# Kernel optimization log

Measured on AMD Instinct MI355X. Metric: run time of the kernel, lower is better.

The kernel has to match this reference:

```python
import jax, jax.numpy as jnp
import numpy as np

W = 8       # token width
H = 2       # attention heads
NC = 1024   # number of cycles
L = 256     # darts per cycle
CLAMP = 10000.0


def _safe(x, clamp=CLAMP):
    x = jnp.nan_to_num(x, nan=0.0, posinf=clamp, neginf=-clamp)
    return jnp.clip(x, -clamp, clamp)


def _safe_softmax(logits, axis):
    w = jax.nn.softmax(_safe(logits), axis=axis)
    w = jnp.nan_to_num(w, nan=0.0, posinf=0.0, neginf=0.0)
    denom = jnp.maximum(w.sum(axis=axis, keepdims=True), 1e-6)
    return w / denom


def _layernorm(x, g, b, eps=1e-5):
    mu = x.mean(-1, keepdims=True)
    var = x.var(-1, keepdims=True)  # biased, matches torch LayerNorm
    return (x - mu) * jax.lax.rsqrt(var + eps) * g + b


def _mha(x, in_w, in_b, out_w, out_b, n_heads, mask=None):
    # torch nn.MultiheadAttention (batch_first) semantics. x: [B,S,E]
    B, S, E = x.shape
    d = E // n_heads
    qkv = x @ in_w.T + in_b
    q, k, v = jnp.split(qkv, 3, axis=-1)
    q = q.reshape(B, S, n_heads, d)
    k = k.reshape(B, S, n_heads, d)
    v = v.reshape(B, S, n_heads, d)
    scores = jnp.einsum('bshd,bthd->bhst', q, k) / jnp.sqrt(jnp.asarray(d, x.dtype))
    if mask is not None:
        scores = scores + mask  # broadcast [S,S] over batch/heads
    attn = jax.nn.softmax(scores, axis=-1)
    out = jnp.einsum('bhst,bthd->bshd', attn, v).reshape(B, S, E)
    return out @ out_w.T + out_b


def _cycle_mask(length):
    m = jnp.full((length, length), -1e9, dtype=jnp.float32)
    i = jnp.arange(length)
    m = m.at[i, i].set(0.0)
    m = m.at[i, (i - 1) % length].set(0.0)
    m = m.at[i, (i + 1) % length].set(0.0)
    return m


def _normalize_orientation(darts):
    # darts: [L,2]; polygon vertices are cumulative sums (origin first, last dart dropped)
    verts = jnp.concatenate([jnp.zeros((1, 2), darts.dtype), jnp.cumsum(darts[:-1], axis=0)], axis=0)
    x, y = verts[:, 0], verts[:, 1]
    area = 0.5 * jnp.sum(x * jnp.roll(y, -1) - y * jnp.roll(x, -1))
    return jnp.where(area >= 0.0, darts, jnp.flip(-darts, axis=0))


def setup_inputs() -> dict:
    key = jax.random.key(0)
    ks = jax.random.split(key, 32)
    def p(i, shape, s=0.2):
        return jax.random.normal(ks[i], shape, jnp.float32) * s
    return {
        'dart_features': jax.random.normal(ks[0], (NC, L, 3), jnp.float32),
        # dart_embed Linear(3,W)
        'de_w': p(1, (W, 3)), 'de_b': p(2, (W,)),
        # cycle_attn MultiheadAttention(W, 2)
        'ca_in_w': p(3, (3 * W, W)), 'ca_in_b': p(4, (3 * W,)),
        'ca_out_w': p(5, (W, W)), 'ca_out_b': p(6, (W,)),
        # cycle_norm
        'cn_g': jnp.ones((W,), jnp.float32), 'cn_b': jnp.zeros((W,), jnp.float32),
        # cycle_score Linear(W,1)
        'cs_w': p(7, (1, W)), 'cs_b': p(8, (1,)),
        # cycle_pool_proj: LN, Linear, ReLU, Linear
        'cp_ln_g': jnp.ones((W,), jnp.float32), 'cp_ln_b': jnp.zeros((W,), jnp.float32),
        'cp_w1': p(9, (W, W)), 'cp_b1': p(10, (W,)),
        'cp_w2': p(11, (W, W)), 'cp_b2': p(12, (W,)),
        # inter_cycle_attn
        'ia_in_w': p(13, (3 * W, W)), 'ia_in_b': p(14, (3 * W,)),
        'ia_out_w': p(15, (W, W)), 'ia_out_b': p(16, (W,)),
        # inter_cycle_norm
        'in_g': jnp.ones((W,), jnp.float32), 'in_b': jnp.zeros((W,), jnp.float32),
        # inter_cycle_score
        'is_w': p(17, (1, W)), 'is_b': p(18, (1,)),
        # token_proj: LN, Linear, ReLU, Linear
        'tp_ln_g': jnp.ones((W,), jnp.float32), 'tp_ln_b': jnp.zeros((W,), jnp.float32),
        'tp_w1': p(19, (W, W)), 'tp_b1': p(20, (W,)),
        'tp_w2': p(21, (W, W)), 'tp_b2': p(22, (W,)),
    }


def reference(dart_features, de_w, de_b, ca_in_w, ca_in_b, ca_out_w, ca_out_b,
              cn_g, cn_b, cs_w, cs_b, cp_ln_g, cp_ln_b, cp_w1, cp_b1, cp_w2, cp_b2,
              ia_in_w, ia_in_b, ia_out_w, ia_out_b, in_g, in_b, is_w, is_b,
              tp_ln_g, tp_ln_b, tp_w1, tp_b1, tp_w2, tp_b2):
    nc, ln, _ = dart_features.shape
    # ---- encode_cycle, vectorized over all cycles ----
    xy = jax.vmap(_normalize_orientation)(dart_features[..., :2])          # [C,L,2]
    nrm = jnp.linalg.norm(xy, axis=-1, keepdims=True)
    feats = _safe(jnp.concatenate([xy, nrm], axis=-1))                     # [C,L,3]
    emb = _safe(jax.nn.relu(feats @ de_w.T + de_b))                        # [C,L,W]
    mask = _cycle_mask(ln)
    attn = _mha(emb, ca_in_w, ca_in_b, ca_out_w, ca_out_b, H, mask)
    emb = _safe(_layernorm(_safe(emb + attn), cn_g, cn_b))                 # [C,L,W]
    logits = _safe((emb @ cs_w.T + cs_b)[..., 0])                          # [C,L]
    wts = _safe_softmax(logits, axis=1)
    pooled = jnp.sum(emb * wts[..., None], axis=1)                         # [C,W]
    hpool = _layernorm(pooled, cp_ln_g, cp_ln_b)
    cyc = _safe(jax.nn.relu(hpool @ cp_w1.T + cp_b1) @ cp_w2.T + cp_b2)    # [C,W]
    # ---- tokenize_collection ----
    coll = _safe(cyc)[None]                                                # [1,C,W]
    attn2 = _mha(coll, ia_in_w, ia_in_b, ia_out_w, ia_out_b, H)
    coll = _safe(_layernorm(_safe(coll + attn2), in_g, in_b))[0]           # [C,W]
    lg = _safe((coll @ is_w.T + is_b)[..., 0])                             # [C]
    w2 = _safe_softmax(lg, axis=0)
    tok_in = jnp.sum(coll * w2[:, None], axis=0)                           # [W]
    h2 = _layernorm(tok_in, tp_ln_g, tp_ln_b)
    token = _safe(jax.nn.relu(h2 @ tp_w1.T + tp_b1) @ tp_w2.T + tp_b2)     # [W]
    return token
```

## Files before the change

kernel.cpp:

```cpp
#include <hip/hip_runtime.h>
#include <math.h>

#define FCLAMP 10000.0f
#define LQ 256
#define NCYC 1024
#define WDIM 8

__device__ __forceinline__ float safef(float x) {
    if (isnan(x)) return 0.0f;
    x = fminf(x, FCLAMP);
    x = fmaxf(x, -FCLAMP);
    return x;
}

__device__ __forceinline__ float wsum_b(float v) {
#pragma unroll
    for (int m = 1; m <= 32; m <<= 1) v += __shfl_xor(v, m, 64);
    return v;
}
__device__ __forceinline__ float wmax_b(float v) {
#pragma unroll
    for (int m = 1; m <= 32; m <<= 1) v = fmaxf(v, __shfl_xor(v, m, 64));
    return v;
}

__global__ __launch_bounds__(LQ) void k_cycle(
    const float* __restrict__ df,
    const float* __restrict__ de_w, const float* __restrict__ de_b,
    const float* __restrict__ ca_in_w, const float* __restrict__ ca_in_b,
    const float* __restrict__ ca_out_w, const float* __restrict__ ca_out_b,
    const float* __restrict__ cn_g, const float* __restrict__ cn_b,
    const float* __restrict__ cs_w, const float* __restrict__ cs_b,
    const float* __restrict__ cp_ln_g, const float* __restrict__ cp_ln_b,
    const float* __restrict__ cp_w1, const float* __restrict__ cp_b1,
    const float* __restrict__ cp_w2, const float* __restrict__ cp_b2,
    const float* __restrict__ ia_in_w, const float* __restrict__ ia_in_b,
    float* __restrict__ ws_cyc,
    float* __restrict__ ws_q,
    float* __restrict__ ws_kT,
    float* __restrict__ ws_vT)
{
    __shared__ float sdx[LQ], sdy[LQ];
    __shared__ float sk[LQ][9], sv[LQ][9];
    __shared__ float swx[4], swy[4];
    __shared__ float sredA[4], sredB[4];
    __shared__ float spool[4][WDIM];

    const int tid  = threadIdx.x;
    const int nc   = blockIdx.x;
    const int lane = tid & 63;
    const int wid  = tid >> 6;

    const float* base = df + (size_t)nc * (LQ * 3);
    const float dx = base[tid * 3 + 0];
    const float dy = base[tid * 3 + 1];
    sdx[tid] = dx; sdy[tid] = dy;

    float ix = dx, iy = dy;
#pragma unroll
    for (int off = 1; off < 64; off <<= 1) {
        const float tx = __shfl_up(ix, off, 64);
        const float ty = __shfl_up(iy, off, 64);
        if (lane >= off) { ix += tx; iy += ty; }
    }
    if (lane == 63) { swx[wid] = ix; swy[wid] = iy; }
    __syncthreads();
    float ox = 0.f, oy = 0.f;
    for (int w = 0; w < wid; ++w) { ox += swx[w]; oy += swy[w]; }
    const float vx = ox + ix - dx;
    const float vy = oy + iy - dy;
    float c = (tid < LQ - 1) ? (vx * dy - vy * dx) : 0.f;
    float s = wsum_b(c);
    if (lane == 0) sredA[wid] = s;
    __syncthreads();
    const float area2 = sredA[0] + sredA[1] + sredA[2] + sredA[3];
    const bool flip = !(area2 >= 0.f);

    float xx, yy;
    if (flip) { xx = -sdx[LQ - 1 - tid]; yy = -sdy[LQ - 1 - tid]; }
    else      { xx =  dx;                yy =  dy; }

    const float fx = safef(xx);
    const float fy = safef(yy);
    const float fn = safef(sqrtf(xx * xx + yy * yy));

    float emb[WDIM];
#pragma unroll
    for (int j = 0; j < WDIM; ++j) {
        float e = de_b[j] + fx * de_w[j * 3 + 0] + fy * de_w[j * 3 + 1] + fn * de_w[j * 3 + 2];
        emb[j] = safef(fmaxf(e, 0.f));
    }

    float q[WDIM], kk[WDIM], vv[WDIM];
#pragma unroll
    for (int o = 0; o < 24; ++o) {
        float val = ca_in_b[o];
#pragma unroll
        for (int k = 0; k < WDIM; ++k) val += emb[k] * ca_in_w[o * WDIM + k];
        if (o < 8)       q[o] = val;
        else if (o < 16) { kk[o - 8]  = val; sk[tid][o - 8]  = val; }
        else             { vv[o - 16] = val; sv[tid][o - 16] = val; }
    }
    __syncthreads();

    const int ip  = (tid + LQ - 1) & (LQ - 1);
    const int inx = (tid + 1) & (LQ - 1);
    float attn8[WDIM];
#pragma unroll
    for (int h = 0; h < 2; ++h) {
        float s0 = 0.f, s1 = 0.f, s2 = 0.f;
#pragma unroll
        for (int d = 0; d < 4; ++d) {
            const float qv = q[h * 4 + d];
            s0 += qv * sk[ip][h * 4 + d];
            s1 += qv * kk[h * 4 + d];
            s2 += qv * sk[inx][h * 4 + d];
        }
        s0 *= 0.5f; s1 *= 0.5f; s2 *= 0.5f;
        const float m  = fmaxf(s0, fmaxf(s1, s2));
        const float e0 = __expf(s0 - m), e1 = __expf(s1 - m), e2 = __expf(s2 - m);
        const float inv = 1.f / (e0 + e1 + e2);
#pragma unroll
        for (int d = 0; d < 4; ++d)
            attn8[h * 4 + d] = (e0 * sv[ip][h * 4 + d] + e1 * vv[h * 4 + d] +
                                e2 * sv[inx][h * 4 + d]) * inv;
    }

    float x8[WDIM];
#pragma unroll
    for (int j = 0; j < WDIM; ++j) {
        float ao = ca_out_b[j];
#pragma unroll
        for (int k = 0; k < WDIM; ++k) ao += attn8[k] * ca_out_w[j * WDIM + k];
        x8[j] = safef(emb[j] + ao);
    }
    float mu = 0.f;
#pragma unroll
    for (int j = 0; j < WDIM; ++j) mu += x8[j];
    mu *= (1.f / WDIM);
    float var = 0.f;
#pragma unroll
    for (int j = 0; j < WDIM; ++j) { const float d = x8[j] - mu; var += d * d; }
    var *= (1.f / WDIM);
    const float rs = rsqrtf(var + 1e-5f);
    float emb2[WDIM];
#pragma unroll
    for (int j = 0; j < WDIM; ++j)
        emb2[j] = safef((x8[j] - mu) * rs * cn_g[j] + cn_b[j]);

    float lg = cs_b[0];
#pragma unroll
    for (int j = 0; j < WDIM; ++j) lg += emb2[j] * cs_w[j];
    lg = safef(lg);

    float wm = wmax_b(lg);
    if (lane == 0) sredB[wid] = wm;
    __syncthreads();
    const float M = fmaxf(fmaxf(sredB[0], sredB[1]), fmaxf(sredB[2], sredB[3]));
    const float e = __expf(lg - M);
    float psum = wsum_b(e);
    if (lane == 0) sredA[wid] = psum;
    __syncthreads();
    const float S = sredA[0] + sredA[1] + sredA[2] + sredA[3];
    const float wgt = e / S;

#pragma unroll
    for (int j = 0; j < WDIM; ++j) {
        const float pj = wsum_b(wgt * emb2[j]);
        if (lane == 0) spool[wid][j] = pj;
    }
    __syncthreads();

    if (wid == 0) {
        const int l8 = lane & 7;
        const float p = spool[0][l8] + spool[1][l8] + spool[2][l8] + spool[3][l8];
        float mu2 = p;
        mu2 += __shfl_xor(mu2, 1, 8); mu2 += __shfl_xor(mu2, 2, 8); mu2 += __shfl_xor(mu2, 4, 8);
        mu2 *= 0.125f;
        const float dd = p - mu2;
        float v2 = dd * dd;
        v2 += __shfl_xor(v2, 1, 8); v2 += __shfl_xor(v2, 2, 8); v2 += __shfl_xor(v2, 4, 8);
        const float rs2 = rsqrtf(v2 * 0.125f + 1e-5f);
        const float hh = dd * rs2 * cp_ln_g[l8] + cp_ln_b[l8];
        float a = cp_b1[l8];
#pragma unroll
        for (int k = 0; k < 8; ++k) a += __shfl(hh, k, 8) * cp_w1[l8 * 8 + k];
        const float r = fmaxf(a, 0.f);
        a = cp_b2[l8];
#pragma unroll
        for (int k = 0; k < 8; ++k) a += __shfl(r, k, 8) * cp_w2[l8 * 8 + k];
        const float cy = safef(a);
        if (lane < 8) ws_cyc[nc * 8 + lane] = cy;
        const int o = (lane < 24) ? lane : 0;
        float g2 = ia_in_b[o];
#pragma unroll
        for (int k = 0; k < 8; ++k) g2 += __shfl(cy, k, 64) * ia_in_w[o * 8 + k];
        if (lane < 8)       ws_q[nc * 8 + lane] = g2;
        else if (lane < 16) ws_kT[(lane - 8) * NCYC + nc] = g2;
        else if (lane < 24) ws_vT[(lane - 16) * NCYC + nc] = g2;
    }
}

__global__ __launch_bounds__(256) void k_token_attn(
    const float* __restrict__ ws_cyc,
    const float* __restrict__ ws_q,
    const float* __restrict__ ws_kT,
    const float* __restrict__ ws_vT,
    const float* __restrict__ ia_out_w, const float* __restrict__ ia_out_b,
    const float* __restrict__ in_g, const float* __restrict__ in_b,
    const float* __restrict__ is_w, const float* __restrict__ is_b,
    float* __restrict__ ws_coll,
    float* __restrict__ ws_lg)
{
    const int lane = threadIdx.x & 63;
    const int wid  = threadIdx.x >> 6;
    const int g    = blockIdx.x * 4 + wid;

    float q[8];
#pragma unroll
    for (int d = 0; d < 8; ++d) q[d] = ws_q[g * 8 + d];

    float sc0[16], sc1[16];
    float m0 = -1e30f, m1 = -1e30f;
#pragma unroll
    for (int j = 0; j < 16; ++j) {
        const int t = (j << 6) | lane;
        float s0 = 0.f, s1 = 0.f;
#pragma unroll
        for (int d = 0; d < 4; ++d) {
            s0 += q[d]     * ws_kT[d * NCYC + t];
            s1 += q[4 + d] * ws_kT[(4 + d) * NCYC + t];
        }
        sc0[j] = s0; sc1[j] = s1;
        m0 = fmaxf(m0, s0); m1 = fmaxf(m1, s1);
    }
    m0 = wmax_b(m0); m1 = wmax_b(m1);

    float l0 = 0.f, l1 = 0.f;
    float a0[4] = {0.f, 0.f, 0.f, 0.f}, a1[4] = {0.f, 0.f, 0.f, 0.f};
#pragma unroll
    for (int j = 0; j < 16; ++j) {
        const int t = (j << 6) | lane;
        const float e0 = __expf(0.5f * (sc0[j] - m0));
        const float e1 = __expf(0.5f * (sc1[j] - m1));
        l0 += e0; l1 += e1;
#pragma unroll
        for (int d = 0; d < 4; ++d) {
            a0[d] += e0 * ws_vT[d * NCYC + t];
            a1[d] += e1 * ws_vT[(4 + d) * NCYC + t];
        }
    }
    l0 = wsum_b(l0); l1 = wsum_b(l1);
#pragma unroll
    for (int d = 0; d < 4; ++d) { a0[d] = wsum_b(a0[d]); a1[d] = wsum_b(a1[d]); }

    float attn8[8];
#pragma unroll
    for (int d = 0; d < 4; ++d) { attn8[d] = a0[d] / l0; attn8[4 + d] = a1[d] / l1; }

    float x8[8];
#pragma unroll
    for (int j = 0; j < 8; ++j) {
        float ao = ia_out_b[j];
#pragma unroll
        for (int k = 0; k < 8; ++k) ao += attn8[k] * ia_out_w[j * 8 + k];
        x8[j] = safef(ws_cyc[g * 8 + j] + ao);
    }
    float mu = 0.f;
#pragma unroll
    for (int j = 0; j < 8; ++j) mu += x8[j];
    mu *= 0.125f;
    float var = 0.f;
#pragma unroll
    for (int j = 0; j < 8; ++j) { const float d = x8[j] - mu; var += d * d; }
    var *= 0.125f;
    const float rs = rsqrtf(var + 1e-5f);
    float lgv = is_b[0];
    float cl8[8];
#pragma unroll
    for (int j = 0; j < 8; ++j) {
        cl8[j] = safef((x8[j] - mu) * rs * in_g[j] + in_b[j]);
        lgv += cl8[j] * is_w[j];
    }
    if (lane == 0) {
#pragma unroll
        for (int j = 0; j < 8; ++j) ws_coll[g * 8 + j] = cl8[j];
        ws_lg[g] = safef(lgv);
    }
}

__global__ __launch_bounds__(NCYC) void k_final(
    const float* __restrict__ ws_coll, const float* __restrict__ ws_lg,
    const float* __restrict__ tp_ln_g, const float* __restrict__ tp_ln_b,
    const float* __restrict__ tp_w1, const float* __restrict__ tp_b1,
    const float* __restrict__ tp_w2, const float* __restrict__ tp_b2,
    float* __restrict__ out)
{
    __shared__ float sredA[16], sredB[16];
    __shared__ float spool[16][8];
    const int tid  = threadIdx.x;
    const int lane = tid & 63;
    const int wid  = tid >> 6;

    const float lg = ws_lg[tid];
    float coll[8];
#pragma unroll
    for (int j = 0; j < 8; ++j) coll[j] = ws_coll[tid * 8 + j];

    float wm = wmax_b(lg);
    if (lane == 0) sredA[wid] = wm;
    __syncthreads();
    float M = sredA[0];
    for (int i = 1; i < 16; ++i) M = fmaxf(M, sredA[i]);
    const float e = __expf(lg - M);
    float ps = wsum_b(e);
    if (lane == 0) sredB[wid] = ps;
    __syncthreads();
    float S = 0.f;
    for (int i = 0; i < 16; ++i) S += sredB[i];
    const float w = e / S;

#pragma unroll
    for (int j = 0; j < 8; ++j) {
        const float pj = wsum_b(w * coll[j]);
        if (lane == 0) spool[wid][j] = pj;
    }
    __syncthreads();

    if (wid == 0) {
        const int l8 = lane & 7;
        float p = 0.f;
        for (int i = 0; i < 16; ++i) p += spool[i][l8];
        float mu = p;
        mu += __shfl_xor(mu, 1, 8); mu += __shfl_xor(mu, 2, 8); mu += __shfl_xor(mu, 4, 8);
        mu *= 0.125f;
        const float dd = p - mu;
        float v2 = dd * dd;
        v2 += __shfl_xor(v2, 1, 8); v2 += __shfl_xor(v2, 2, 8); v2 += __shfl_xor(v2, 4, 8);
        const float rs = rsqrtf(v2 * 0.125f + 1e-5f);
        const float h = dd * rs * tp_ln_g[l8] + tp_ln_b[l8];
        float a = tp_b1[l8];
#pragma unroll
        for (int k = 0; k < 8; ++k) a += __shfl(h, k, 8) * tp_w1[l8 * 8 + k];
        const float r = fmaxf(a, 0.f);
        a = tp_b2[l8];
#pragma unroll
        for (int k = 0; k < 8; ++k) a += __shfl(r, k, 8) * tp_w2[l8 * 8 + k];
        if (lane < 8) out[lane] = safef(a);
    }
}

extern "C" void kernel_launch(void* const* d_in, const int* in_sizes, int n_in,
                              void* d_out, int out_size, void* d_ws, size_t ws_size,
                              hipStream_t stream) {
    const float* df       = (const float*)d_in[0];
    const float* de_w     = (const float*)d_in[1];
    const float* de_b     = (const float*)d_in[2];
    const float* ca_in_w  = (const float*)d_in[3];
    const float* ca_in_b  = (const float*)d_in[4];
    const float* ca_out_w = (const float*)d_in[5];
    const float* ca_out_b = (const float*)d_in[6];
    const float* cn_g     = (const float*)d_in[7];
    const float* cn_b     = (const float*)d_in[8];
    const float* cs_w     = (const float*)d_in[9];
    const float* cs_b     = (const float*)d_in[10];
    const float* cp_ln_g  = (const float*)d_in[11];
    const float* cp_ln_b  = (const float*)d_in[12];
    const float* cp_w1    = (const float*)d_in[13];
    const float* cp_b1    = (const float*)d_in[14];
    const float* cp_w2    = (const float*)d_in[15];
    const float* cp_b2    = (const float*)d_in[16];
    const float* ia_in_w  = (const float*)d_in[17];
    const float* ia_in_b  = (const float*)d_in[18];
    const float* ia_out_w = (const float*)d_in[19];
    const float* ia_out_b = (const float*)d_in[20];
    const float* in_g     = (const float*)d_in[21];
    const float* in_b     = (const float*)d_in[22];
    const float* is_w     = (const float*)d_in[23];
    const float* is_b     = (const float*)d_in[24];
    const float* tp_ln_g  = (const float*)d_in[25];
    const float* tp_ln_b  = (const float*)d_in[26];
    const float* tp_w1    = (const float*)d_in[27];
    const float* tp_b1    = (const float*)d_in[28];
    const float* tp_w2    = (const float*)d_in[29];
    const float* tp_b2    = (const float*)d_in[30];

    float* ws      = (float*)d_ws;
    float* ws_cyc  = ws;
    float* ws_q    = ws + NCYC * 8;
    float* ws_kT   = ws + NCYC * 16;
    float* ws_vT   = ws + NCYC * 24;
    float* ws_coll = ws + NCYC * 32;
    float* ws_lg   = ws + NCYC * 40;

    k_cycle<<<NCYC, LQ, 0, stream>>>(
        df, de_w, de_b, ca_in_w, ca_in_b, ca_out_w, ca_out_b,
        cn_g, cn_b, cs_w, cs_b, cp_ln_g, cp_ln_b,
        cp_w1, cp_b1, cp_w2, cp_b2, ia_in_w, ia_in_b,
        ws_cyc, ws_q, ws_kT, ws_vT);

    k_token_attn<<<NCYC / 4, 256, 0, stream>>>(
        ws_cyc, ws_q, ws_kT, ws_vT, ia_out_w, ia_out_b, in_g, in_b, is_w, is_b,
        ws_coll, ws_lg);

    k_final<<<1, NCYC, 0, stream>>>(
        ws_coll, ws_lg, tp_ln_g, tp_ln_b, tp_w1, tp_b1, tp_w2, tp_b2,
        (float*)d_out);
}
```

Baseline: 135.7 us.

## Use one wavefront per cycle and fuse the final reduction via a last-block atomic

Measured after the change: 149.0 us (median of 2 runs). +9.8%, slower.

```diff
diff --git a/kernel.cpp b/kernel.cpp
--- a/kernel.cpp
+++ b/kernel.cpp
@@ -2,15 +2,12 @@
 #include <math.h>
 
 #define FCLAMP 10000.0f
-#define LQ 256
 #define NCYC 1024
-#define WDIM 8
+#define NB2 (NCYC / 4)
 
 __device__ __forceinline__ float safef(float x) {
     if (isnan(x)) return 0.0f;
-    x = fminf(x, FCLAMP);
-    x = fmaxf(x, -FCLAMP);
-    return x;
+    return fmaxf(fminf(x, FCLAMP), -FCLAMP);
 }
 
 __device__ __forceinline__ float wsum_b(float v) {
@@ -24,7 +21,7 @@
     return v;
 }
 
-__global__ __launch_bounds__(LQ) void k_cycle(
+__global__ __launch_bounds__(64, 1) void k_cycle(
     const float* __restrict__ df,
     const float* __restrict__ de_w, const float* __restrict__ de_b,
     const float* __restrict__ ca_in_w, const float* __restrict__ ca_in_b,
@@ -38,170 +35,206 @@
     float* __restrict__ ws_cyc,
     float* __restrict__ ws_q,
     float* __restrict__ ws_kT,
-    float* __restrict__ ws_vT)
+    float* __restrict__ ws_vT,
+    unsigned* __restrict__ ws_cnt)
 {
-    __shared__ float sdx[LQ], sdy[LQ];
-    __shared__ float sk[LQ][9], sv[LQ][9];
-    __shared__ float swx[4], swy[4];
-    __shared__ float sredA[4], sredB[4];
-    __shared__ float spool[4][WDIM];
-
-    const int tid  = threadIdx.x;
+    const int lane = threadIdx.x;
     const int nc   = blockIdx.x;
-    const int lane = tid & 63;
-    const int wid  = tid >> 6;
-
-    const float* base = df + (size_t)nc * (LQ * 3);
-    const float dx = base[tid * 3 + 0];
-    const float dy = base[tid * 3 + 1];
-    sdx[tid] = dx; sdy[tid] = dy;
-
-    float ix = dx, iy = dy;
+    if (nc == 0 && lane == 0) *ws_cnt = 0u;
+
+    const float* base = df + (size_t)nc * 768 + lane * 12;
+    const float4 A = *(const float4*)(base);
+    const float4 B = *(const float4*)(base + 4);
+    const float4 C = *(const float4*)(base + 8);
+    float dxr[4] = {A.x, A.w, B.z, C.y};
+    float dyr[4] = {A.y, B.x, B.w, C.z};
+
+    float sx[4], sy[4];
+    sx[0] = dxr[0]; sy[0] = dyr[0];
+#pragma unroll
+    for (int r = 1; r < 4; ++r) { sx[r] = sx[r - 1] + dxr[r]; sy[r] = sy[r - 1] + dyr[r]; }
+    const float tx = sx[3], ty = sy[3];
+    float ixs = tx, iys = ty;
 #pragma unroll
     for (int off = 1; off < 64; off <<= 1) {
-        const float tx = __shfl_up(ix, off, 64);
-        const float ty = __shfl_up(iy, off, 64);
-        if (lane >= off) { ix += tx; iy += ty; }
-    }
-    if (lane == 63) { swx[wid] = ix; swy[wid] = iy; }
-    __syncthreads();
-    float ox = 0.f, oy = 0.f;
-    for (int w = 0; w < wid; ++w) { ox += swx[w]; oy += swy[w]; }
-    const float vx = ox + ix - dx;
-    const float vy = oy + iy - dy;
-    float c = (tid < LQ - 1) ? (vx * dy - vy * dx) : 0.f;
-    float s = wsum_b(c);
-    if (lane == 0) sredA[wid] = s;
-    __syncthreads();
-    const float area2 = sredA[0] + sredA[1] + sredA[2] + sredA[3];
-    const bool flip = !(area2 >= 0.f);
-
-    float xx, yy;
-    if (flip) { xx = -sdx[LQ - 1 - tid]; yy = -sdy[LQ - 1 - tid]; }
-    else      { xx =  dx;                yy =  dy; }
-
-    const float fx = safef(xx);
-    const float fy = safef(yy);
-    const float fn = safef(sqrtf(xx * xx + yy * yy));
-
-    float emb[WDIM];
-#pragma unroll
-    for (int j = 0; j < WDIM; ++j) {
-        float e = de_b[j] + fx * de_w[j * 3 + 0] + fy * de_w[j * 3 + 1] + fn * de_w[j * 3 + 2];
-        emb[j] = safef(fmaxf(e, 0.f));
-    }
-
-    float q[WDIM], kk[WDIM], vv[WDIM];
-#pragma unroll
-    for (int o = 0; o < 24; ++o) {
-        float val = ca_in_b[o];
-#pragma unroll
-        for (int k = 0; k < WDIM; ++k) val += emb[k] * ca_in_w[o * WDIM + k];
-        if (o < 8)       q[o] = val;
-        else if (o < 16) { kk[o - 8]  = val; sk[tid][o - 8]  = val; }
-        else             { vv[o - 16] = val; sv[tid][o - 16] = val; }
-    }
-    __syncthreads();
-
-    const int ip  = (tid + LQ - 1) & (LQ - 1);
-    const int inx = (tid + 1) & (LQ - 1);
-    float attn8[WDIM];
-#pragma unroll
-    for (int h = 0; h < 2; ++h) {
-        float s0 = 0.f, s1 = 0.f, s2 = 0.f;
-#pragma unroll
-        for (int d = 0; d < 4; ++d) {
-            const float qv = q[h * 4 + d];
-            s0 += qv * sk[ip][h * 4 + d];
-            s1 += qv * kk[h * 4 + d];
-            s2 += qv * sk[inx][h * 4 + d];
-        }
-        s0 *= 0.5f; s1 *= 0.5f; s2 *= 0.5f;
-        const float m  = fmaxf(s0, fmaxf(s1, s2));
-        const float e0 = __expf(s0 - m), e1 = __expf(s1 - m), e2 = __expf(s2 - m);
-        const float inv = 1.f / (e0 + e1 + e2);
-#pragma unroll
-        for (int d = 0; d < 4; ++d)
-            attn8[h * 4 + d] = (e0 * sv[ip][h * 4 + d] + e1 * vv[h * 4 + d] +
-                                e2 * sv[inx][h * 4 + d]) * inv;
-    }
-
-    float x8[WDIM];
-#pragma unroll
-    for (int j = 0; j < WDIM; ++j) {
-        float ao = ca_out_b[j];
-#pragma unroll
-        for (int k = 0; k < WDIM; ++k) ao += attn8[k] * ca_out_w[j * WDIM + k];
-        x8[j] = safef(emb[j] + ao);
-    }
-    float mu = 0.f;
-#pragma unroll
-    for (int j = 0; j < WDIM; ++j) mu += x8[j];
-    mu *= (1.f / WDIM);
-    float var = 0.f;
-#pragma unroll
-    for (int j = 0; j < WDIM; ++j) { const float d = x8[j] - mu; var += d * d; }
-    var *= (1.f / WDIM);
-    const float rs = rsqrtf(var + 1e-5f);
-    float emb2[WDIM];
-#pragma unroll
-    for (int j = 0; j < WDIM; ++j)
-        emb2[j] = safef((x8[j] - mu) * rs * cn_g[j] + cn_b[j]);
-
-    float lg = cs_b[0];
-#pragma unroll
-    for (int j = 0; j < WDIM; ++j) lg += emb2[j] * cs_w[j];
-    lg = safef(lg);
-
-    float wm = wmax_b(lg);
-    if (lane == 0) sredB[wid] = wm;
-    __syncthreads();
-    const float M = fmaxf(fmaxf(sredB[0], sredB[1]), fmaxf(sredB[2], sredB[3]));
-    const float e = __expf(lg - M);
-    float psum = wsum_b(e);
-    if (lane == 0) sredA[wid] = psum;
-    __syncthreads();
-    const float S = sredA[0] + sredA[1] + sredA[2] + sredA[3];
-    const float wgt = e / S;
-
-#pragma unroll
-    for (int j = 0; j < WDIM; ++j) {
-        const float pj = wsum_b(wgt * emb2[j]);
-        if (lane == 0) spool[wid][j] = pj;
-    }
-    __syncthreads();
-
-    if (wid == 0) {
-        const int l8 = lane & 7;
-        const float p = spool[0][l8] + spool[1][l8] + spool[2][l8] + spool[3][l8];
-        float mu2 = p;
-        mu2 += __shfl_xor(mu2, 1, 8); mu2 += __shfl_xor(mu2, 2, 8); mu2 += __shfl_xor(mu2, 4, 8);
-        mu2 *= 0.125f;
-        const float dd = p - mu2;
-        float v2 = dd * dd;
-        v2 += __shfl_xor(v2, 1, 8); v2 += __shfl_xor(v2, 2, 8); v2 += __shfl_xor(v2, 4, 8);
-        const float rs2 = rsqrtf(v2 * 0.125f + 1e-5f);
-        const float hh = dd * rs2 * cp_ln_g[l8] + cp_ln_b[l8];
-        float a = cp_b1[l8];
-#pragma unroll
-        for (int k = 0; k < 8; ++k) a += __shfl(hh, k, 8) * cp_w1[l8 * 8 + k];
-        const float r = fmaxf(a, 0.f);
-        a = cp_b2[l8];
-#pragma unroll
-        for (int k = 0; k < 8; ++k) a += __shfl(r, k, 8) * cp_w2[l8 * 8 + k];
-        const float cy = safef(a);
-        if (lane < 8) ws_cyc[nc * 8 + lane] = cy;
-        const int o = (lane < 24) ? lane : 0;
-        float g2 = ia_in_b[o];
-#pragma unroll
-        for (int k = 0; k < 8; ++k) g2 += __shfl(cy, k, 64) * ia_in_w[o * 8 + k];
+        const float ax = __shfl_up(ixs, off, 64);
+        const float ay = __shfl_up(iys, off, 64);
+        if (lane >= off) { ixs += ax; iys += ay; }
+    }
+    const float bx = ixs - tx, by = iys - ty;
+
+    float cc = 0.f;
+#pragma unroll
+    for (int r = 0; r < 4; ++r) {
+        const float vx = bx + (r ? sx[r - 1] : 0.f);
+        const float vy = by + (r ? sy[r - 1] : 0.f);
+        if ((lane * 4 + r) < 255) cc += vx * dyr[r] - vy * dxr[r];
+    }
+    const float area2 = wsum_b(cc);
+
+    if (!(area2 >= 0.f)) {
+        float nx[4], ny[4];
+#pragma unroll
+        for (int r = 0; r < 4; ++r) {
+            nx[r] = -__shfl(dxr[3 - r], 63 - lane, 64);
+            ny[r] = -__shfl(dyr[3 - r], 63 - lane, 64);
+        }
+#pragma unroll
+        for (int r = 0; r < 4; ++r) { dxr[r] = nx[r]; dyr[r] = ny[r]; }
+    }
+
+    float embA[4][8];
+#pragma unroll
+    for (int r = 0; r < 4; ++r) {
+        const float fx = safef(dxr[r]);
+        const float fy = safef(dyr[r]);
+        const float fn = safef(sqrtf(dxr[r] * dxr[r] + dyr[r] * dyr[r]));
+#pragma unroll
+        for (int j = 0; j < 8; ++j) {
+            const float e = de_b[j] + fx * de_w[j * 3] + fy * de_w[j * 3 + 1] + fn * de_w[j * 3 + 2];
+            embA[r][j] = safef(fmaxf(e, 0.f));
+        }
+    }
+
+    float qA[4][8], kA[4][8], vA[4][8];
+#pragma unroll
+    for (int r = 0; r < 4; ++r) {
+#pragma unroll
+        for (int o = 0; o < 24; ++o) {
+            float val = ca_in_b[o];
+#pragma unroll
+            for (int k = 0; k < 8; ++k) val += embA[r][k] * ca_in_w[o * 8 + k];
+            if (o < 8)       qA[r][o] = val;
+            else if (o < 16) kA[r][o - 8] = val;
+            else             vA[r][o - 16] = val;
+        }
+    }
+
+    const int lprev = (lane + 63) & 63, lnext = (lane + 1) & 63;
+    float kp[8], kn[8], vp[8], vn[8];
+#pragma unroll
+    for (int d = 0; d < 8; ++d) {
+        kp[d] = __shfl(kA[3][d], lprev, 64);
+        kn[d] = __shfl(kA[0][d], lnext, 64);
+        vp[d] = __shfl(vA[3][d], lprev, 64);
+        vn[d] = __shfl(vA[0][d], lnext, 64);
+    }
+
+    float lgr[4];
+#pragma unroll
+    for (int r = 0; r < 4; ++r) {
+        float kprev[8], knext[8], vprev[8], vnext[8];
+#pragma unroll
+        for (int d = 0; d < 8; ++d) {
+            kprev[d] = (r == 0) ? kp[d] : kA[r - 1][d];
+            knext[d] = (r == 3) ? kn[d] : kA[r + 1][d];
+            vprev[d] = (r == 0) ? vp[d] : vA[r - 1][d];
+            vnext[d] = (r == 3) ? vn[d] : vA[r + 1][d];
+        }
+        float att[8];
+#pragma unroll
+        for (int h = 0; h < 2; ++h) {
+            float s0 = 0.f, s1 = 0.f, s2 = 0.f;
+#pragma unroll
+            for (int d = 0; d < 4; ++d) {
+                const float qv = qA[r][h * 4 + d];
+                s0 += qv * kprev[h * 4 + d];
+                s1 += qv * kA[r][h * 4 + d];
+                s2 += qv * knext[h * 4 + d];
+            }
+            s0 *= 0.5f; s1 *= 0.5f; s2 *= 0.5f;
+            const float m  = fmaxf(s0, fmaxf(s1, s2));
+            const float e0 = __expf(s0 - m), e1 = __expf(s1 - m), e2 = __expf(s2 - m);
+            const float inv = 1.f / (e0 + e1 + e2);
+#pragma unroll
+            for (int d = 0; d < 4; ++d)
+                att[h * 4 + d] = (e0 * vprev[h * 4 + d] + e1 * vA[r][h * 4 + d] +
+                                  e2 * vnext[h * 4 + d]) * inv;
+        }
+        float x8[8];
+#pragma unroll
+        for (int j = 0; j < 8; ++j) {
+            float ao = ca_out_b[j];
+#pragma unroll
+            for (int k = 0; k < 8; ++k) ao += att[k] * ca_out_w[j * 8 + k];
+            x8[j] = safef(embA[r][j] + ao);
+        }
+        float mu = 0.f;
+#pragma unroll
+        for (int j = 0; j < 8; ++j) mu += x8[j];
+        mu *= 0.125f;
+        float var = 0.f;
+#pragma unroll
+        for (int j = 0; j < 8; ++j) { const float d = x8[j] - mu; var += d * d; }
+        var *= 0.125f;
+        const float rs = rsqrtf(var + 1e-5f);
+        float lg = cs_b[0];
+#pragma unroll
+        for (int j = 0; j < 8; ++j) {
+            embA[r][j] = safef((x8[j] - mu) * rs * cn_g[j] + cn_b[j]);
+            lg += embA[r][j] * cs_w[j];
+        }
+        lgr[r] = safef(lg);
+    }
+
+    float M = fmaxf(fmaxf(lgr[0], lgr[1]), fmaxf(lgr[2], lgr[3]));
+    M = wmax_b(M);
+    float er[4], esum = 0.f;
+#pragma unroll
+    for (int r = 0; r < 4; ++r) { er[r] = __expf(lgr[r] - M); esum += er[r]; }
+    const float S = wsum_b(esum);
+    const float invS = 1.f / S;
+    float pool[8];
+#pragma unroll
+    for (int j = 0; j < 8; ++j) {
+        float pj = er[0] * embA[0][j] + er[1] * embA[1][j] + er[2] * embA[2][j] + er[3] * embA[3][j];
+        pool[j] = wsum_b(pj) * invS;
+    }
+
+    float mu2 = 0.f;
+#pragma unroll
+    for (int j = 0; j < 8; ++j) mu2 += pool[j];
+    mu2 *= 0.125f;
+    float v2 = 0.f;
+#pragma unroll
+    for (int j = 0; j < 8; ++j) { const float d = pool[j] - mu2; v2 += d * d; }
+    const float rs2 = rsqrtf(v2 * 0.125f + 1e-5f);
+    float hh[8];
+#pragma unroll
+    for (int j = 0; j < 8; ++j) hh[j] = (pool[j] - mu2) * rs2 * cp_ln_g[j] + cp_ln_b[j];
+    float r1[8];
+#pragma unroll
+    for (int j = 0; j < 8; ++j) {
+        float a = cp_b1[j];
+#pragma unroll
+        for (int k = 0; k < 8; ++k) a += hh[k] * cp_w1[j * 8 + k];
+        r1[j] = fmaxf(a, 0.f);
+    }
+    float cy[8];
+#pragma unroll
+    for (int j = 0; j < 8; ++j) {
+        float a = cp_b2[j];
+#pragma unroll
+        for (int k = 0; k < 8; ++k) a += r1[k] * cp_w2[j * 8 + k];
+        cy[j] = safef(a);
+    }
+    if (lane == 0) {
+        *(float4*)(ws_cyc + nc * 8)     = make_float4(cy[0], cy[1], cy[2], cy[3]);
+        *(float4*)(ws_cyc + nc * 8 + 4) = make_float4(cy[4], cy[5], cy[6], cy[7]);
+    }
+
+    if (lane < 24) {
+        const float* wrow = ia_in_w + lane * 8;
+        float g2 = ia_in_b[lane];
+#pragma unroll
+        for (int k = 0; k < 8; ++k) g2 += cy[k] * wrow[k];
         if (lane < 8)       ws_q[nc * 8 + lane] = g2;
         else if (lane < 16) ws_kT[(lane - 8) * NCYC + nc] = g2;
-        else if (lane < 24) ws_vT[(lane - 16) * NCYC + nc] = g2;
-    }
-}
-
-__global__ __launch_bounds__(256) void k_token_attn(
+        else                ws_vT[(lane - 16) * NCYC + nc] = g2;
+    }
+}
+
+__global__ __launch_bounds__(256) void k_attn_final(
     const float* __restrict__ ws_cyc,
     const float* __restrict__ ws_q,
     const float* __restrict__ ws_kT,
@@ -209,45 +242,64 @@
     const float* __restrict__ ia_out_w, const float* __restrict__ ia_out_b,
     const float* __restrict__ in_g, const float* __restrict__ in_b,
     const float* __restrict__ is_w, const float* __restrict__ is_b,
+    const float* __restrict__ tp_ln_g, const float* __restrict__ tp_ln_b,
+    const float* __restrict__ tp_w1, const float* __restrict__ tp_b1,
+    const float* __restrict__ tp_w2, const float* __restrict__ tp_b2,
     float* __restrict__ ws_coll,
-    float* __restrict__ ws_lg)
+    float* __restrict__ ws_lg,
+    unsigned* __restrict__ ws_cnt,
+    float* __restrict__ out)
 {
+    __shared__ float sredM[4], sredS[4], spool[4][8];
+    __shared__ unsigned s_last;
+
     const int lane = threadIdx.x & 63;
     const int wid  = threadIdx.x >> 6;
     const int g    = blockIdx.x * 4 + wid;
 
     float q[8];
 #pragma unroll
-    for (int d = 0; d < 8; ++d) q[d] = ws_q[g * 8 + d];
+    for (int d = 0; d < 8; ++d) q[d] = 0.5f * ws_q[g * 8 + d];
 
     float sc0[16], sc1[16];
     float m0 = -1e30f, m1 = -1e30f;
 #pragma unroll
-    for (int j = 0; j < 16; ++j) {
-        const int t = (j << 6) | lane;
-        float s0 = 0.f, s1 = 0.f;
+    for (int j = 0; j < 4; ++j) {
+        const int t4 = j * 256 + lane * 4;
+        float s0[4] = {0, 0, 0, 0}, s1[4] = {0, 0, 0, 0};
+#pragma unroll
+        for (int d = 0; d < 8; ++d) {
+            const float4 kv = *(const float4*)(ws_kT + d * NCYC + t4);
+            const float qd = q[d];
+            float* s = (d < 4) ? s0 : s1;
+            s[0] += qd * kv.x; s[1] += qd * kv.y; s[2] += qd * kv.z; s[3] += qd * kv.w;
+        }
+#pragma unroll
+        for (int c = 0; c < 4; ++c) {
+            sc0[j * 4 + c] = s0[c]; sc1[j * 4 + c] = s1[c];
+            m0 = fmaxf(m0, s0[c]); m1 = fmaxf(m1, s1[c]);
+        }
+    }
+    m0 = wmax_b(m0); m1 = wmax_b(m1);
+
+    float l0 = 0.f, l1 = 0.f;
+    float a0[4] = {0, 0, 0, 0}, a1[4] = {0, 0, 0, 0};
+#pragma unroll
+    for (int j = 0; j < 4; ++j) {
+        const int t4 = j * 256 + lane * 4;
+        float e0[4], e1[4];
+#pragma unroll
+        for (int c = 0; c < 4; ++c) {
+            e0[c] = __expf(sc0[j * 4 + c] - m0);
+            e1[c] = __expf(sc1[j * 4 + c] - m1);
+            l0 += e0[c]; l1 += e1[c];
+        }
 #pragma unroll
         for (int d = 0; d < 4; ++d) {
-            s0 += q[d]     * ws_kT[d * NCYC + t];
-            s1 += q[4 + d] * ws_kT[(4 + d) * NCYC + t];
-        }
-        sc0[j] = s0; sc1[j] = s1;
-        m0 = fmaxf(m0, s0); m1 = fmaxf(m1, s1);
-    }
-    m0 = wmax_b(m0); m1 = wmax_b(m1);
-
-    float l0 = 0.f, l1 = 0.f;
-    float a0[4] = {0.f, 0.f, 0.f, 0.f}, a1[4] = {0.f, 0.f, 0.f, 0.f};
-#pragma unroll
-    for (int j = 0; j < 16; ++j) {
-        const int t = (j << 6) | lane;
-        const float e0 = __expf(0.5f * (sc0[j] - m0));
-        const float e1 = __expf(0.5f * (sc1[j] - m1));
-        l0 += e0; l1 += e1;
-#pragma unroll
-        for (int d = 0; d < 4; ++d) {
-            a0[d] += e0 * ws_vT[d * NCYC + t];
-            a1[d] += e1 * ws_vT[(4 + d) * NCYC + t];
+            const float4 v0 = *(const float4*)(ws_vT + d * NCYC + t4);
+            const float4 v1 = *(const float4*)(ws_vT + (4 + d) * NCYC + t4);
+            a0[d] += e0[0] * v0.x + e0[1] * v0.y + e0[2] * v0.z + e0[3] * v0.w;
+            a1[d] += e1[0] * v1.x + e1[1] * v1.y + e1[2] * v1.z + e1[3] * v1.w;
         }
     }
     l0 = wsum_b(l0); l1 = wsum_b(l1);
@@ -258,13 +310,16 @@
 #pragma unroll
     for (int d = 0; d < 4; ++d) { attn8[d] = a0[d] / l0; attn8[4 + d] = a1[d] / l1; }
 
+    const float4 cyA = *(const float4*)(ws_cyc + g * 8);
+    const float4 cyB = *(const float4*)(ws_cyc + g * 8 + 4);
+    const float cyc[8] = {cyA.x, cyA.y, cyA.z, cyA.w, cyB.x, cyB.y, cyB.z, cyB.w};
     float x8[8];
 #pragma unroll
     for (int j = 0; j < 8; ++j) {
         float ao = ia_out_b[j];
 #pragma unroll
         for (int k = 0; k < 8; ++k) ao += attn8[k] * ia_out_w[j * 8 + k];
-        x8[j] = safef(ws_cyc[g * 8 + j] + ao);
+        x8[j] = safef(cyc[j] + ao);
     }
     float mu = 0.f;
 #pragma unroll
@@ -283,70 +338,85 @@
         lgv += cl8[j] * is_w[j];
     }
     if (lane == 0) {
-#pragma unroll
-        for (int j = 0; j < 8; ++j) ws_coll[g * 8 + j] = cl8[j];
+        *(float4*)(ws_coll + g * 8)     = make_float4(cl8[0], cl8[1], cl8[2], cl8[3]);
+        *(float4*)(ws_coll + g * 8 + 4) = make_float4(cl8[4], cl8[5], cl8[6], cl8[7]);
         ws_lg[g] = safef(lgv);
     }
-}
-
-__global__ __launch_bounds__(NCYC) void k_final(
-    const float* __restrict__ ws_coll, const float* __restrict__ ws_lg,
-    const float* __restrict__ tp_ln_g, const float* __restrict__ tp_ln_b,
-    const float* __restrict__ tp_w1, const float* __restrict__ tp_b1,
-    const float* __restrict__ tp_w2, const float* __restrict__ tp_b2,
-    float* __restrict__ out)
-{
-    __shared__ float sredA[16], sredB[16];
-    __shared__ float spool[16][8];
-    const int tid  = threadIdx.x;
-    const int lane = tid & 63;
-    const int wid  = tid >> 6;
-
-    const float lg = ws_lg[tid];
-    float coll[8];
-#pragma unroll
-    for (int j = 0; j < 8; ++j) coll[j] = ws_coll[tid * 8 + j];
-
-    float wm = wmax_b(lg);
-    if (lane == 0) sredA[wid] = wm;
+
     __syncthreads();
-    float M = sredA[0];
-    for (int i = 1; i < 16; ++i) M = fmaxf(M, sredA[i]);
-    const float e = __expf(lg - M);
-    float ps = wsum_b(e);
-    if (lane == 0) sredB[wid] = ps;
+    if (threadIdx.x == 0) {
+        __threadfence();
+        const unsigned old = atomicAdd(ws_cnt, 1u);
+        s_last = (old == NB2 - 1) ? 1u : 0u;
+    }
     __syncthreads();
-    float S = 0.f;
-    for (int i = 0; i < 16; ++i) S += sredB[i];
-    const float w = e / S;
-
-#pragma unroll
-    for (int j = 0; j < 8; ++j) {
-        const float pj = wsum_b(w * coll[j]);
+    if (!s_last) return;
+    __threadfence();
+
+    const int tid = threadIdx.x;
+    float lgv4[4], cl[4][8];
+#pragma unroll
+    for (int r = 0; r < 4; ++r) {
+        const int t = tid + 256 * r;
+        lgv4[r] = ws_lg[t];
+        const float4 u = *(const float4*)(ws_coll + t * 8);
+        const float4 w = *(const float4*)(ws_coll + t * 8 + 4);
+        cl[r][0] = u.x; cl[r][1] = u.y; cl[r][2] = u.z; cl[r][3] = u.w;
+        cl[r][4] = w.x; cl[r][5] = w.y; cl[r][6] = w.z; cl[r][7] = w.w;
+    }
+    float m = fmaxf(fmaxf(lgv4[0], lgv4[1]), fmaxf(lgv4[2], lgv4[3]));
+    m = wmax_b(m);
+    if (lane == 0) sredM[wid] = m;
+    __syncthreads();
+    const float M = fmaxf(fmaxf(sredM[0], sredM[1]), fmaxf(sredM[2], sredM[3]));
+    float er[4], es = 0.f;
+#pragma unroll
+    for (int r = 0; r < 4; ++r) { er[r] = __expf(lgv4[r] - M); es += er[r]; }
+    es = wsum_b(es);
+    if (lane == 0) sredS[wid] = es;
+#pragma unroll
+    for (int j = 0; j < 8; ++j) {
+        float pj = er[0] * cl[0][j] + er[1] * cl[1][j] + er[2] * cl[2][j] + er[3] * cl[3][j];
+        pj = wsum_b(pj);
         if (lane == 0) spool[wid][j] = pj;
     }
     __syncthreads();
 
     if (wid == 0) {
-        const int l8 = lane & 7;
-        float p = 0.f;
-        for (int i = 0; i < 16; ++i) p += spool[i][l8];
-        float mu = p;
-        mu += __shfl_xor(mu, 1, 8); mu += __shfl_xor(mu, 2, 8); mu += __shfl_xor(mu, 4, 8);
-        mu *= 0.125f;
-        const float dd = p - mu;
-        float v2 = dd * dd;
-        v2 += __shfl_xor(v2, 1, 8); v2 += __shfl_xor(v2, 2, 8); v2 += __shfl_xor(v2, 4, 8);
-        const float rs = rsqrtf(v2 * 0.125f + 1e-5f);
-        const float h = dd * rs * tp_ln_g[l8] + tp_ln_b[l8];
-        float a = tp_b1[l8];
-#pragma unroll
-        for (int k = 0; k < 8; ++k) a += __shfl(h, k, 8) * tp_w1[l8 * 8 + k];
-        const float r = fmaxf(a, 0.f);
-        a = tp_b2[l8];
-#pragma unroll
-        for (int k = 0; k < 8; ++k) a += __shfl(r, k, 8) * tp_w2[l8 * 8 + k];
-        if (lane < 8) out[lane] = safef(a);
+        const float S = sredS[0] + sredS[1] + sredS[2] + sredS[3];
+        const float invS = 1.f / S;
+        float pool[8];
+#pragma unroll
+        for (int j = 0; j < 8; ++j)
+            pool[j] = (spool[0][j] + spool[1][j] + spool[2][j] + spool[3][j]) * invS;
+        float mu2 = 0.f;
+#pragma unroll
+        for (int j = 0; j < 8; ++j) mu2 += pool[j];
+        mu2 *= 0.125f;
+        float v2 = 0.f;
+#pragma unroll
+        for (int j = 0; j < 8; ++j) { const float d = pool[j] - mu2; v2 += d * d; }
+        const float rs2 = rsqrtf(v2 * 0.125f + 1e-5f);
+        float hh[8];
+#pragma unroll
+        for (int j = 0; j < 8; ++j) hh[j] = (pool[j] - mu2) * rs2 * tp_ln_g[j] + tp_ln_b[j];
+        float r1[8];
+#pragma unroll
+        for (int j = 0; j < 8; ++j) {
+            float a = tp_b1[j];
+#pragma unroll
+            for (int k = 0; k < 8; ++k) a += hh[k] * tp_w1[j * 8 + k];
+            r1[j] = fmaxf(a, 0.f);
+        }
+        if (lane == 0) {
+#pragma unroll
+            for (int j = 0; j < 8; ++j) {
+                float a = tp_b2[j];
+#pragma unroll
+                for (int k = 0; k < 8; ++k) a += r1[k] * tp_w2[j * 8 + k];
+                out[j] = safef(a);
+            }
+        }
     }
 }
 
@@ -392,18 +462,16 @@
     float* ws_vT   = ws + NCYC * 24;
     float* ws_coll = ws + NCYC * 32;
     float* ws_lg   = ws + NCYC * 40;
-
-    k_cycle<<<NCYC, LQ, 0, stream>>>(
+    unsigned* ws_cnt = (unsigned*)(ws + NCYC * 41);
+
+    k_cycle<<<NCYC, 64, 0, stream>>>(
         df, de_w, de_b, ca_in_w, ca_in_b, ca_out_w, ca_out_b,
         cn_g, cn_b, cs_w, cs_b, cp_ln_g, cp_ln_b,
         cp_w1, cp_b1, cp_w2, cp_b2, ia_in_w, ia_in_b,
-        ws_cyc, ws_q, ws_kT, ws_vT);
-
-    k_token_attn<<<NCYC / 4, 256, 0, stream>>>(
+        ws_cyc, ws_q, ws_kT, ws_vT, ws_cnt);
+
+    k_attn_final<<<NB2, 256, 0, stream>>>(
         ws_cyc, ws_q, ws_kT, ws_vT, ia_out_w, ia_out_b, in_g, in_b, is_w, is_b,
-        ws_coll, ws_lg);
-
-    k_final<<<1, NCYC, 0, stream>>>(
-        ws_coll, ws_lg, tp_ln_g, tp_ln_b, tp_w1, tp_b1, tp_w2, tp_b2,
-        (float*)d_out);
-}
+        tp_ln_g, tp_ln_b, tp_w1, tp_b1, tp_w2, tp_b2,
+        ws_coll, ws_lg, ws_cnt, (float*)d_out);
+}
```
